# Optimization experiments

Hardware: AMD Instinct MI355X
Metric: run time of the kernel (lower is better)

## Reference

```python
import jax, jax.numpy as jnp
import numpy as np

B, FRAMES, IMG, PATCH = 2, 4, 224, 16
D_MODEL, D_INNER, D_STATE, DT_RANK, DEPTH, D_CONV = 256, 512, 16, 16, 12, 4
NPATCH = (IMG // PATCH) ** 2  # 196


def setup_inputs() -> dict:
    keys = iter(jax.random.split(jax.random.key(0), 80))

    def n(shape, s=0.02):
        return jax.random.normal(next(keys), shape, dtype=jnp.float32) * s

    A_init = jnp.broadcast_to(jnp.log(jnp.arange(1, D_STATE + 1, dtype=jnp.float32)), (DEPTH, D_INNER, D_STATE))
    inp = {
        'x': jax.random.normal(next(keys), (B, 3, FRAMES, IMG, IMG), dtype=jnp.float32),
        'patch_w': n((D_MODEL, 3, 1, PATCH, PATCH)),
        'patch_b': jnp.zeros((D_MODEL,), jnp.float32),
        'pos_embed': n((1, NPATCH, D_MODEL)),
        'temp_pos': n((1, FRAMES, D_MODEL)),
        'in_proj_w': n((DEPTH, 2 * D_INNER, D_MODEL), D_MODEL ** -0.5),
        'convf_w': n((DEPTH, D_INNER, D_CONV), 0.3),
        'convf_b': jnp.zeros((DEPTH, D_INNER), jnp.float32),
        'xprojf_w': n((DEPTH, DT_RANK + 2 * D_STATE, D_INNER), D_INNER ** -0.5),
        'dtf_w': n((DEPTH, D_INNER, DT_RANK), DT_RANK ** -0.5),
        'dtf_b': jnp.full((DEPTH, D_INNER), -4.6, jnp.float32) + n((DEPTH, D_INNER), 0.1),
        'A_logf': A_init,
        'Dsf': jnp.ones((DEPTH, D_INNER), jnp.float32),
        'convb_w': n((DEPTH, D_INNER, D_CONV), 0.3),
        'convb_b': jnp.zeros((DEPTH, D_INNER), jnp.float32),
        'xprojb_w': n((DEPTH, DT_RANK + 2 * D_STATE, D_INNER), D_INNER ** -0.5),
        'dtb_w': n((DEPTH, D_INNER, DT_RANK), DT_RANK ** -0.5),
        'dtb_b': jnp.full((DEPTH, D_INNER), -4.6, jnp.float32) + n((DEPTH, D_INNER), 0.1),
        'A_logb': A_init,
        'Dsb': jnp.ones((DEPTH, D_INNER), jnp.float32),
        'out_proj_w': n((DEPTH, D_MODEL, D_INNER), D_INNER ** -0.5),
        'norm_w': jnp.ones((DEPTH, D_MODEL), jnp.float32),
        'normf_w': jnp.ones((D_MODEL,), jnp.float32),
        'bbox_w1': n((D_MODEL, D_MODEL), D_MODEL ** -0.5),
        'bbox_b1': jnp.zeros((D_MODEL,), jnp.float32),
        'bbox_w2': n((3, D_MODEL), D_MODEL ** -0.5),
        'bbox_b2': jnp.zeros((3,), jnp.float32),
        'pix_w1': n((4, D_MODEL, D_MODEL), D_MODEL ** -0.5),
        'pix_b1': jnp.zeros((4, D_MODEL), jnp.float32),
        'pix_w2': n((4, 2, D_MODEL), D_MODEL ** -0.5),
        'pix_b2': jnp.zeros((4, 2), jnp.float32),
    }
    return inp


def rmsnorm(x, w, eps=1e-5):
    x = x.astype(jnp.float32)
    return x * jax.lax.rsqrt(jnp.mean(x * x, axis=-1, keepdims=True) + eps) * w


def ssm_scan(u, dt, A, Bm, Cm):
    # u, dt: [B,L,di]; Bm, Cm: [B,L,st]; A: [di,st]
    def step(h, inp):
        dt_t, B_t, C_t, u_t = inp  # [B,di],[B,st],[B,st],[B,di]
        h = jnp.exp(dt_t[..., None] * A) * h + (dt_t * u_t)[..., None] * B_t[:, None, :]
        return h, jnp.einsum('bds,bs->bd', h, C_t)
    h0 = jnp.zeros((u.shape[0], u.shape[2], A.shape[1]), u.dtype)
    xs = (dt.swapaxes(0, 1), Bm.swapaxes(0, 1), Cm.swapaxes(0, 1), u.swapaxes(0, 1))
    _, ys = jax.lax.scan(step, h0, xs)
    return ys.swapaxes(0, 1)  # [B,L,di]


def mamba_dir(x, z, cw, cb, xpw, dtw, dtb, A_log, Ds):
    L = x.shape[1]
    xp = jnp.pad(x, ((0, 0), (D_CONV - 1, 0), (0, 0)))  # causal depthwise conv
    xc = cb + sum(xp[:, k:k + L, :] * cw[:, k] for k in range(D_CONV))
    xs = jax.nn.silu(xc)
    dbl = xs @ xpw.T  # [B,L,dt_rank+2*st]
    dt = jax.nn.softplus(dbl[..., :DT_RANK] @ dtw.T + dtb)
    Bm = dbl[..., DT_RANK:DT_RANK + D_STATE]
    Cm = dbl[..., DT_RANK + D_STATE:]
    y = ssm_scan(xs, dt, -jnp.exp(A_log), Bm, Cm) + Ds * xs
    return y * jax.nn.silu(z)


def _forward(x, patch_w, patch_b, pos_embed, temp_pos, in_proj_w, convf_w, convf_b, xprojf_w, dtf_w, dtf_b, A_logf, Dsf, convb_w, convb_b, xprojb_w, dtb_w, dtb_b, A_logb, Dsb, out_proj_w, norm_w, normf_w, bbox_w1, bbox_b1, bbox_w2, bbox_b2, pix_w1, pix_b1, pix_w2, pix_b2):
    feat = jax.lax.conv_general_dilated(x, patch_w, (1, PATCH, PATCH), 'VALID', dimension_numbers=('NCDHW', 'OIDHW', 'NCDHW'))
    feat = feat + patch_b[None, :, None, None, None]
    b, c, t, h, w = feat.shape
    np_ = h * w
    tok = feat.transpose(0, 2, 3, 4, 1).reshape(b * t, np_, c) + pos_embed
    tok = tok.reshape(b, t, np_, c).transpose(0, 2, 1, 3).reshape(b * np_, t, c) + temp_pos
    tok = tok.reshape(b, np_, t, c).transpose(0, 2, 1, 3).reshape(b, t * np_, c)
    hidden, residual = tok, None
    for i in range(DEPTH):
        residual = hidden if residual is None else hidden + residual  # fused add+norm (prenorm)
        hidden = rmsnorm(residual, norm_w[i])
        xz = hidden @ in_proj_w[i].T
        xi, zi = jnp.split(xz, 2, axis=-1)
        yf = mamba_dir(xi, zi, convf_w[i], convf_b[i], xprojf_w[i], dtf_w[i], dtf_b[i], A_logf[i], Dsf[i])
        yb = mamba_dir(xi[:, ::-1], zi[:, ::-1], convb_w[i], convb_b[i], xprojb_w[i], dtb_w[i], dtb_b[i], A_logb[i], Dsb[i])[:, ::-1]
        hidden = (yf + yb) @ out_proj_w[i].T
    residual = hidden + residual
    hidden = rmsnorm(residual, normf_w)
    fus = hidden[:, :5, :]  # [B,5,hidden_dim] fusion_output for DETR head
    bbox = jax.nn.relu(fus[:, 0] @ bbox_w1.T + bbox_b1) @ bbox_w2.T + bbox_b2  # [B,3]
    pix = jnp.stack([jax.nn.sigmoid(jax.nn.relu(fus[:, i + 1] @ pix_w1[i].T + pix_b1[i]) @ pix_w2[i].T + pix_b2[i]) for i in range(4)], axis=1)  # [B,4,2]
    return jnp.concatenate([bbox, pix.reshape(bbox.shape[0], 8)], axis=-1)  # [B,11]


def reference(x, patch_w, patch_b, pos_embed, temp_pos, in_proj_w, convf_w, convf_b, xprojf_w, dtf_w, dtf_b, A_logf, Dsf, convb_w, convb_b, xprojb_w, dtb_w, dtb_b, A_logb, Dsb, out_proj_w, norm_w, normf_w, bbox_w1, bbox_b1, bbox_w2, bbox_b2, pix_w1, pix_b1, pix_w2, pix_b2):
    return _forward(x, patch_w, patch_b, pos_embed, temp_pos, in_proj_w, convf_w, convf_b, xprojf_w, dtf_w, dtf_b, A_logf, Dsf, convb_w, convb_b, xprojb_w, dtb_w, dtb_b, A_logb, Dsb, out_proj_w, norm_w, normf_w, bbox_w1, bbox_b1, bbox_w2, bbox_b2, pix_w1, pix_b1, pix_w2, pix_b2)
```

## Files before the change

kernel.cpp:

```cpp
#include <hip/hip_runtime.h>
#include <hip/hip_bf16.h>
#include <cmath>

#define BB 2
#define TT 4
#define NPATCH 196
#define LL 784
#define CC 256
#define DI 512
#define NSTATE 16
#define DEPTH 12
#define NCHUNK 49
#define CLEN 16
#define CTAU 8

typedef short short8 __attribute__((ext_vector_type(8)));
typedef float f32x4 __attribute__((ext_vector_type(4)));

__device__ __forceinline__ float sigmoidf_(float x){ return 1.f/(1.f+__expf(-x)); }
__device__ __forceinline__ float siluf_(float x){ return x/(1.f+__expf(-x)); }
__device__ __forceinline__ float softplusf_(float x){ return x > 20.f ? x : log1pf(__expf(x)); }
__device__ __forceinline__ unsigned short f2bf(float f){
  union { float f; unsigned int u; } v; v.f = f;
  unsigned int u = v.u;
  return (unsigned short)((u + 0x7FFFu + ((u>>16)&1u)) >> 16);
}
__device__ __forceinline__ float bf2f(unsigned short u){
  union { unsigned int i; float f; } v; v.i = ((unsigned int)u)<<16; return v.f;
}

#define PREP_NA 3072
#define PREP_NB 1536
#define PREP_NC 192
#define PREP_ND 1536
#define PREP_NF 784
#define PREP_NG 4704
__global__ void k_prep_all(
    const float* __restrict__ in_proj, unsigned short* __restrict__ WinB,
    const float* __restrict__ out_proj, unsigned short* __restrict__ WoutB,
    const float* __restrict__ patch_w, unsigned short* __restrict__ WpB,
    const float* __restrict__ xpf, const float* __restrict__ xpb, unsigned short* __restrict__ Wxp,
    const float* __restrict__ pb, const float* __restrict__ pos, const float* __restrict__ tpos,
    float* __restrict__ PB,
    const float* __restrict__ x, unsigned short* __restrict__ XCol)
{
  int blk = blockIdx.x;
  if (blk < PREP_NA + PREP_NB + PREP_NC) {
    const float* src; unsigned short* dst; int i;
    if (blk < PREP_NA)                  { src = in_proj;  dst = WinB;  i = blk*256 + threadIdx.x; }
    else if (blk < PREP_NA + PREP_NB)   { src = out_proj; dst = WoutB; i = (blk-PREP_NA)*256 + threadIdx.x; }
    else                                { src = patch_w;  dst = WpB;   i = (blk-PREP_NA-PREP_NB)*256 + threadIdx.x; }
    float4 v = *(const float4*)(src + (size_t)i*4);
    unsigned short o[4] = { f2bf(v.x), f2bf(v.y), f2bf(v.z), f2bf(v.w) };
    *(uint2*)(dst + (size_t)i*4) = *(uint2*)o;
    return;
  }
  blk -= PREP_NA + PREP_NB + PREP_NC;
  if (blk < PREP_ND) {
    int r = blk & 63; int ld = blk >> 6;
    int layer = ld >> 1, dir = ld & 1;
    const float* src = dir ? xpb : xpf;
    for (int kk = threadIdx.x; kk < 512; kk += 256) {
      float v = (r < 48) ? src[((size_t)layer*48 + r)*512 + kk] : 0.f;
      Wxp[((size_t)blk)*512 + kk] = f2bf(v);
    }
    return;
  }
  blk -= PREP_ND;
  if (blk < PREP_NF) {
    int tp = blk;
    int t = tp / NPATCH, p = tp - t*NPATCH;
    int c = threadIdx.x;
    PB[(size_t)tp*CC + c] = pb[c] + pos[(size_t)p*CC + c] + tpos[(size_t)t*CC + c];
    return;
  }
  blk -= PREP_NF;
  {
    int ci = blk / (BB*LL);
    int row = blk - ci*(BB*LL);
    int b = row / LL, rem = row - b*LL;
    int t = rem / NPATCH, p = rem - t*NPATCH;
    int ph = p / 14, pc = p - ph*14;
    int ii = threadIdx.x >> 4, jj = threadIdx.x & 15;
    float v = x[(((size_t)(b*3+ci)*TT + t)*224 + (ph*16+ii))*224 + (pc*16+jj)];
    XCol[(size_t)row*768 + ci*256 + threadIdx.x] = f2bf(v);
  }
}

__global__ __launch_bounds__(256) void k_gemm_mfma(
    const unsigned short* __restrict__ Ab, const unsigned short* __restrict__ Ab2,
    const unsigned short* __restrict__ Wb,
    float* __restrict__ Out, unsigned short* __restrict__ Outb,
    const float* __restrict__ bias, int M, int Nn, int K)
{
  __shared__ short As[64][40];
  __shared__ short Bs[64][40];
  int bm = blockIdx.x*64, bn = blockIdx.y*64;
  int tid = threadIdx.x;
  int wave = tid>>6, lane = tid&63;
  int wm = (wave>>1)*32, wn = (wave&1)*32;
  int quad = lane>>4, l16 = lane&15;
  f32x4 acc[2][2];
  #pragma unroll
  for (int i=0;i<2;i++)
    #pragma unroll
    for (int j=0;j<2;j++){ acc[i][j][0]=0.f; acc[i][j][1]=0.f; acc[i][j][2]=0.f; acc[i][j][3]=0.f; }
  int sr = tid>>2, sc = (tid&3)<<3;
  int gr = bm + sr;
  for (int k0 = 0; k0 < K; k0 += 32) {
    short8 av = {0,0,0,0,0,0,0,0};
    if (gr < M) {
      av = *(const short8*)(Ab + (size_t)gr*K + k0 + sc);
      if (Ab2) {
        short8 a2v = *(const short8*)(Ab2 + (size_t)gr*K + k0 + sc);
        #pragma unroll
        for (int j=0;j<8;j++)
          av[j] = (short)f2bf(bf2f((unsigned short)av[j]) + bf2f((unsigned short)a2v[j]));
      }
    }
    *(short8*)&As[sr][sc] = av;
    short8 bv = *(const short8*)(Wb + (size_t)(bn+sr)*K + k0 + sc);
    *(short8*)&Bs[sr][sc] = bv;
    __syncthreads();
    short8 a0 = *(const short8*)&As[wm    +l16][quad<<3];
    short8 a1 = *(const short8*)&As[wm+16+l16][quad<<3];
    short8 b0 = *(const short8*)&Bs[wn    +l16][quad<<3];
    short8 b1 = *(const short8*)&Bs[wn+16+l16][quad<<3];
    acc[0][0] = __builtin_amdgcn_mfma_f32_16x16x32_bf16(a0,b0,acc[0][0],0,0,0);
    acc[0][1] = __builtin_amdgcn_mfma_f32_16x16x32_bf16(a0,b1,acc[0][1],0,0,0);
    acc[1][0] = __builtin_amdgcn_mfma_f32_16x16x32_bf16(a1,b0,acc[1][0],0,0,0);
    acc[1][1] = __builtin_amdgcn_mfma_f32_16x16x32_bf16(a1,b1,acc[1][1],0,0,0);
    __syncthreads();
  }
  #pragma unroll
  for (int i=0;i<2;i++){
    #pragma unroll
    for (int r=0;r<4;r++){
      int row = bm + wm + i*16 + quad*4 + r;
      if (row < M) {
        #pragma unroll
        for (int j=0;j<2;j++){
          int col = bn + wn + j*16 + l16;
          float vv = acc[i][j][r];
          if (bias) vv += bias[(size_t)(row % LL)*Nn + col];
          if (Outb) Outb[(size_t)row*Nn + col] = f2bf(vv);
          else      Out [(size_t)row*Nn + col] = vv;
        }
      }
    }
  }
}

__global__ __launch_bounds__(256) void k_gemm_xp(
    const unsigned short* __restrict__ XSb, const unsigned short* __restrict__ Wxp,
    float* __restrict__ DBL)
{
  __shared__ short As[64][40];
  __shared__ short Bs[64][40];
  int z = blockIdx.z;
  int bm = blockIdx.x*64;
  const unsigned short* A = XSb + (size_t)z*2*LL*DI;
  const unsigned short* W = Wxp + (size_t)z*64*DI;
  int tid = threadIdx.x;
  int wave = tid>>6, lane = tid&63;
  int wm = (wave>>1)*32, wn = (wave&1)*32;
  int quad = lane>>4, l16 = lane&15;
  f32x4 acc[2][2];
  #pragma unroll
  for (int i=0;i<2;i++)
    #pragma unroll
    for (int j=0;j<2;j++){ acc[i][j][0]=0.f; acc[i][j][1]=0.f; acc[i][j][2]=0.f; acc[i][j][3]=0.f; }
  int sr = tid>>2, sc = (tid&3)<<3;
  int gr = bm + sr;
  for (int k0 = 0; k0 < DI; k0 += 32) {
    short8 av = {0,0,0,0,0,0,0,0};
    if (gr < 2*LL) av = *(const short8*)(A + (size_t)gr*DI + k0 + sc);
    *(short8*)&As[sr][sc] = av;
    *(short8*)&Bs[sr][sc] = *(const short8*)(W + (size_t)sr*DI + k0 + sc);
    __syncthreads();
    short8 a0 = *(const short8*)&As[wm    +l16][quad<<3];
    short8 a1 = *(const short8*)&As[wm+16+l16][quad<<3];
    short8 b0 = *(const short8*)&Bs[wn    +l16][quad<<3];
    short8 b1 = *(const short8*)&Bs[wn+16+l16][quad<<3];
    acc[0][0] = __builtin_amdgcn_mfma_f32_16x16x32_bf16(a0,b0,acc[0][0],0,0,0);
    acc[0][1] = __builtin_amdgcn_mfma_f32_16x16x32_bf16(a0,b1,acc[0][1],0,0,0);
    acc[1][0] = __builtin_amdgcn_mfma_f32_16x16x32_bf16(a1,b0,acc[1][0],0,0,0);
    acc[1][1] = __builtin_amdgcn_mfma_f32_16x16x32_bf16(a1,b1,acc[1][1],0,0,0);
    __syncthreads();
  }
  #pragma unroll
  for (int i=0;i<2;i++){
    #pragma unroll
    for (int r=0;r<4;r++){
      int row = bm + wm + i*16 + quad*4 + r;
      if (row < 2*LL) {
        size_t grow = (size_t)z*2*LL + row;
        #pragma unroll
        for (int j=0;j<2;j++){
          int col = wn + j*16 + l16;
          DBL[grow*64 + col] = acc[i][j][r];
        }
      }
    }
  }
}

__global__ void k_conv_silu(const unsigned short* __restrict__ XZb,
    const float* __restrict__ cwf, const float* __restrict__ cbf,
    const float* __restrict__ cwb, const float* __restrict__ cbb,
    unsigned short* __restrict__ XSb)
{
  int dir = blockIdx.z;
  int blk = blockIdx.x;
  int b = blk / (LL/CTAU), tq = blk - b*(LL/CTAU);
  int t0 = tq * CTAU;
  const float* cw = dir ? cwb : cwf;
  const float* cb = dir ? cbb : cbf;
  int d = threadIdx.x;
  float4 w4 = *(const float4*)(cw + (size_t)d*4);
  float bia = cb[d];
  const unsigned short* xz = XZb + (size_t)b*LL*1024 + d;
  float x0 = 0.f, x1 = 0.f, x2 = 0.f;
  {
    int tt = t0-3; if (tt >= 0) x0 = bf2f(xz[(size_t)(dir ? (LL-1-tt) : tt)*1024]);
    tt = t0-2;     if (tt >= 0) x1 = bf2f(xz[(size_t)(dir ? (LL-1-tt) : tt)*1024]);
    tt = t0-1;     if (tt >= 0) x2 = bf2f(xz[(size_t)(dir ? (LL-1-tt) : tt)*1024]);
  }
  size_t rowbase = ((size_t)(dir*BB + b)*LL + t0)*DI + d;
  #pragma unroll
  for (int i = 0; i < CTAU; ++i) {
    int tt = t0 + i;
    int torig = dir ? (LL-1-tt) : tt;
    float xin = bf2f(xz[(size_t)torig*1024]);
    float acc = bia;
    acc = fmaf(x0, w4.x, acc);
    acc = fmaf(x1, w4.y, acc);
    acc = fmaf(x2, w4.z, acc);
    acc = fmaf(xin, w4.w, acc);
    XSb[rowbase + (size_t)i*DI] = f2bf(siluf_(acc));
    x0 = x1; x1 = x2; x2 = xin;
  }
}

__global__ void k_res_rms(const float* __restrict__ Hin, float* __restrict__ R,
                          unsigned short* __restrict__ Nout, const float* __restrict__ w, int first)
{
  int row = blockIdx.x, c = threadIdx.x;
  size_t idx = (size_t)row*CC + c;
  float h = Hin[idx];
  float r = first ? h : (h + R[idx]);
  R[idx] = r;
  float v = r*r;
  #pragma unroll
  for (int m=1;m<64;m<<=1) v += __shfl_xor(v,m);
  __shared__ float sred[4];
  if ((c & 63)==0) sred[c>>6]=v;
  __syncthreads();
  float tot = sred[0]+sred[1]+sred[2]+sred[3];
  float sc = rsqrtf(tot*(1.f/CC) + 1e-5f);
  Nout[idx] = f2bf(r*sc*w[c]);
}

__global__ void k_scan1(const unsigned short* __restrict__ XSb, const float* __restrict__ DBL,
                        const float* __restrict__ dtwf, const float* __restrict__ dtwb,
                        const float* __restrict__ dtbf, const float* __restrict__ dtbb,
                        const float* __restrict__ Alf, const float* __restrict__ Alb,
                        float* __restrict__ Pb, float* __restrict__ Hcb)
{
  int chunk = blockIdx.x;
  int d = blockIdx.y*256 + threadIdx.x;
  int dirb = blockIdx.z;
  int dir = dirb >> 1;
  const float* Al = dir ? Alb : Alf;
  const float* dtw = dir ? dtwb : dtwf;
  float dtbv = (dir ? dtbb : dtbf)[d];
  float a2[NSTATE], wd[NSTATE];
  {
    const float4* ar = (const float4*)(Al + (size_t)d*NSTATE);
    const float4* wr = (const float4*)(dtw + (size_t)d*NSTATE);
    #pragma unroll
    for (int q=0;q<4;q++){
      float4 v = ar[q];
      a2[q*4+0] = -__expf(v.x)*1.44269504f;
      a2[q*4+1] = -__expf(v.y)*1.44269504f;
      a2[q*4+2] = -__expf(v.z)*1.44269504f;
      a2[q*4+3] = -__expf(v.w)*1.44269504f;
      float4 w = wr[q];
      wd[q*4+0] = w.x; wd[q*4+1] = w.y; wd[q*4+2] = w.z; wd[q*4+3] = w.w;
    }
  }
  __shared__ float Dl[CLEN][NSTATE], Bl[CLEN][NSTATE];
  {
    int t = threadIdx.x >> 4, s = threadIdx.x & 15;
    size_t row = ((size_t)dirb*LL + chunk*CLEN + t)*64;
    Dl[t][s] = DBL[row + s];
    Bl[t][s] = DBL[row + 16 + s];
  }
  __syncthreads();
  size_t base = (size_t)dirb*LL*DI;
  const unsigned short* xs = XSb + base + (size_t)chunk*CLEN*DI + d;
  float P[NSTATE], h[NSTATE];
  #pragma unroll
  for (int s=0;s<NSTATE;s++){ P[s]=1.f; h[s]=0.f; }
  for (int i = 0; i < CLEN; ++i) {
    float dtv = dtbv;
    #pragma unroll
    for (int r=0;r<NSTATE;r++) dtv = fmaf(Dl[i][r], wd[r], dtv);
    float dt = softplusf_(dtv);
    float u  = bf2f(xs[(size_t)i*DI]);
    float du = dt*u;
    #pragma unroll
    for (int s=0;s<NSTATE;s++){
      float e = exp2f(dt*a2[s]);
      P[s] *= e;
      h[s] = fmaf(e, h[s], du*Bl[i][s]);
    }
  }
  size_t ob = ((size_t)dirb*NCHUNK + chunk)*NSTATE*DI + d;
  #pragma unroll
  for (int s=0;s<NSTATE;s++){
    Pb [ob + (size_t)s*DI] = P[s];
    Hcb[ob + (size_t)s*DI] = h[s];
  }
}

__global__ void k_scan2(const float* __restrict__ Pb, float* __restrict__ Hcb)
{
  int i = blockIdx.x*256 + threadIdx.x;
  int dirb = blockIdx.y;
  float h = 0.f;
  for (int c = 0; c < NCHUNK; ++c) {
    size_t idx = ((size_t)dirb*NCHUNK + c)*NSTATE*DI + i;
    float p = Pb[idx], hl = Hcb[idx];
    Hcb[idx] = h;
    h = fmaf(p, h, hl);
  }
}

__global__ void k_scan3(const unsigned short* __restrict__ XSb, const float* __restrict__ DBL,
                        const unsigned short* __restrict__ XZb,
                        const float* __restrict__ dtwf, const float* __restrict__ dtwb,
                        const float* __restrict__ dtbf, const float* __restrict__ dtbb,
                        const float* __restrict__ Alf, const float* __restrict__ Alb,
                        const float* __restrict__ Dsfp, const float* __restrict__ Dsbp,
                        const float* __restrict__ Hcb, unsigned short* __restrict__ Yb)
{
  int chunk = blockIdx.x;
  int d = blockIdx.y*256 + threadIdx.x;
  int dirb = blockIdx.z;
  int dir = dirb >> 1, b = dirb & 1;
  const float* Al = dir ? Alb : Alf;
  const float* dtw = dir ? dtwb : dtwf;
  float dtbv = (dir ? dtbb : dtbf)[d];
  float a2[NSTATE], wd[NSTATE];
  {
    const float4* ar = (const float4*)(Al + (size_t)d*NSTATE);
    const float4* wr = (const float4*)(dtw + (size_t)d*NSTATE);
    #pragma unroll
    for (int q=0;q<4;q++){
      float4 v = ar[q];
      a2[q*4+0] = -__expf(v.x)*1.44269504f;
      a2[q*4+1] = -__expf(v.y)*1.44269504f;
      a2[q*4+2] = -__expf(v.z)*1.44269504f;
      a2[q*4+3] = -__expf(v.w)*1.44269504f;
      float4 w = wr[q];
      wd[q*4+0] = w.x; wd[q*4+1] = w.y; wd[q*4+2] = w.z; wd[q*4+3] = w.w;
    }
  }
  __shared__ float Dl[CLEN][NSTATE];
  __shared__ float BCl[CLEN][32];
  {
    int t = threadIdx.x >> 4, s = threadIdx.x & 15;
    size_t row = ((size_t)dirb*LL + chunk*CLEN + t)*64;
    Dl[t][s] = DBL[row + s];
    BCl[t][s] = DBL[row + 16 + s];
    BCl[t][16+s] = DBL[row + 32 + s];
  }
  __syncthreads();
  float h[NSTATE];
  size_t ob = ((size_t)dirb*NCHUNK + chunk)*NSTATE*DI + d;
  #pragma unroll
  for (int s=0;s<NSTATE;s++) h[s] = Hcb[ob + (size_t)s*DI];
  float Dsv = (dir ? Dsbp : Dsfp)[d];
  size_t base = (size_t)dirb*LL*DI;
  const unsigned short* xs = XSb + base + (size_t)chunk*CLEN*DI + d;
  const unsigned short* zpb = XZb + (size_t)b*LL*1024 + 512 + d;
  unsigned short* y = Yb + base + d;
  for (int i = 0; i < CLEN; ++i) {
    int tau = chunk*CLEN + i;
    float dtv = dtbv;
    #pragma unroll
    for (int r=0;r<NSTATE;r++) dtv = fmaf(Dl[i][r], wd[r], dtv);
    float dt = softplusf_(dtv);
    float u  = bf2f(xs[(size_t)i*DI]);
    float du = dt*u;
    float yacc = 0.f;
    #pragma unroll
    for (int s=0;s<NSTATE;s++){
      float e = exp2f(dt*a2[s]);
      h[s] = fmaf(e, h[s], du*BCl[i][s]);
      yacc = fmaf(h[s], BCl[i][16+s], yacc);
    }
    int torig = dir ? (LL-1-tau) : tau;
    float zv = bf2f(zpb[(size_t)torig*1024]);
    y[(size_t)torig*DI] = f2bf((yacc + Dsv*u) * siluf_(zv));
  }
}

__global__ void k_head(const float* __restrict__ H, const float* __restrict__ R,
                       const float* __restrict__ nw,
                       const float* __restrict__ bw1, const float* __restrict__ bb1,
                       const float* __restrict__ bw2, const float* __restrict__ bb2,
                       const float* __restrict__ pw1, const float* __restrict__ pb1,
                       const float* __restrict__ pw2, const float* __restrict__ pb2,
                       float* __restrict__ out)
{
  int b = blockIdx.x / 5, j = blockIdx.x % 5;
  int c = threadIdx.x;
  __shared__ float fus[CC], h1[CC];
  __shared__ float sred[4];
  size_t idx = ((size_t)b*LL + j)*CC + c;
  float r = H[idx] + R[idx];
  float v = r*r;
  #pragma unroll
  for (int m=1;m<64;m<<=1) v += __shfl_xor(v,m);
  if ((c&63)==0) sred[c>>6]=v;
  __syncthreads();
  float tot = sred[0]+sred[1]+sred[2]+sred[3];
  fus[c] = r * rsqrtf(tot*(1.f/CC)+1e-5f) * nw[c];
  __syncthreads();
  const float* W1 = (j==0) ? bw1 : (pw1 + (size_t)(j-1)*CC*CC);
  const float* B1 = (j==0) ? bb1 : (pb1 + (j-1)*CC);
  float a = B1[c];
  for (int k=0;k<CC;k++) a = fmaf(fus[k], W1[(size_t)c*CC+k], a);
  h1[c] = fmaxf(a, 0.f);
  __syncthreads();
  if (j==0) {
    if (c < 3) {
      float o = bb2[c];
      for (int k=0;k<CC;k++) o = fmaf(h1[k], bw2[c*CC+k], o);
      out[b*11 + c] = o;
    }
  } else {
    if (c < 2) {
      const float* W2 = pw2 + (size_t)((j-1)*2 + c)*CC;
      float o = pb2[(j-1)*2 + c];
      for (int k=0;k<CC;k++) o = fmaf(h1[k], W2[k], o);
      out[b*11 + 3 + (j-1)*2 + c] = sigmoidf_(o);
    }
  }
}

extern "C" void kernel_launch(void* const* d_in, const int* in_sizes, int n_in,
                              void* d_out, int out_size, void* d_ws, size_t ws_size,
                              hipStream_t stream)
{
  const float* x        = (const float*)d_in[0];
  const float* patch_w  = (const float*)d_in[1];
  const float* patch_b  = (const float*)d_in[2];
  const float* pos      = (const float*)d_in[3];
  const float* tpos     = (const float*)d_in[4];
  const float* in_proj  = (const float*)d_in[5];
  const float* convf_w  = (const float*)d_in[6];
  const float* convf_b  = (const float*)d_in[7];
  const float* xprojf_w = (const float*)d_in[8];
  const float* dtf_w    = (const float*)d_in[9];
  const float* dtf_b    = (const float*)d_in[10];
  const float* A_logf   = (const float*)d_in[11];
  const float* Dsf      = (const float*)d_in[12];
  const float* convb_w  = (const float*)d_in[13];
  const float* convb_b  = (const float*)d_in[14];
  const float* xprojb_w = (const float*)d_in[15];
  const float* dtb_w    = (const float*)d_in[16];
  const float* dtb_b    = (const float*)d_in[17];
  const float* A_logb   = (const float*)d_in[18];
  const float* Dsb      = (const float*)d_in[19];
  const float* out_proj = (const float*)d_in[20];
  const float* norm_w   = (const float*)d_in[21];
  const float* normf_w  = (const float*)d_in[22];
  const float* bbox_w1  = (const float*)d_in[23];
  const float* bbox_b1  = (const float*)d_in[24];
  const float* bbox_w2  = (const float*)d_in[25];
  const float* bbox_b2  = (const float*)d_in[26];
  const float* pix_w1   = (const float*)d_in[27];
  const float* pix_b1   = (const float*)d_in[28];
  const float* pix_w2   = (const float*)d_in[29];
  const float* pix_b2   = (const float*)d_in[30];
  float* out = (float*)d_out;

  float* ws = (float*)d_ws;
  const size_t nTok = (size_t)BB*LL;
  float* H   = ws;                 ws += nTok*CC;
  float* R   = ws;                 ws += nTok*CC;
  float* DBL = ws;                 ws += 2*nTok*64;
  float* Pb  = ws;                 ws += (size_t)4*NCHUNK*NSTATE*DI;
  float* Hcb = ws;                 ws += (size_t)4*NCHUNK*NSTATE*DI;
  float* PB  = ws;                 ws += (size_t)LL*CC;
  unsigned short* WinB  = (unsigned short*)ws;  ws += (size_t)DEPTH*1024*CC/2;
  unsigned short* WoutB = (unsigned short*)ws;  ws += (size_t)DEPTH*CC*DI/2;
  unsigned short* WpB   = (unsigned short*)ws;  ws += (size_t)CC*768/2;
  unsigned short* XCol  = (unsigned short*)ws;  ws += nTok*768/2;
  unsigned short* NrmB  = (unsigned short*)ws;  ws += nTok*CC/2;
  unsigned short* XZb   = (unsigned short*)ws;  ws += nTok*1024/2;
  unsigned short* XSb   = (unsigned short*)ws;  ws += 2*nTok*DI/2;
  unsigned short* Yb    = (unsigned short*)ws;  ws += 2*nTok*DI/2;
  unsigned short* Wxp   = (unsigned short*)ws;  ws += (size_t)DEPTH*2*64*DI/2;
  (void)ws_size; (void)in_sizes; (void)n_in; (void)out_size;

  {
    const unsigned prepBlocks = PREP_NA + PREP_NB + PREP_NC + PREP_ND + PREP_NF + PREP_NG;
    k_prep_all<<<dim3(prepBlocks), 256, 0, stream>>>(
        in_proj, WinB, out_proj, WoutB, patch_w, WpB,
        xprojf_w, xprojb_w, Wxp,
        patch_b, pos, tpos, PB, x, XCol);
  }
  k_gemm_mfma<<<dim3(25, 4), 256, 0, stream>>>(XCol, nullptr, WpB, H, nullptr, PB,
                                               (int)nTok, CC, 768);

  for (int i = 0; i < DEPTH; ++i) {
    k_res_rms<<<dim3((unsigned)nTok), 256, 0, stream>>>(H, R, NrmB, norm_w + i*CC, i==0 ? 1 : 0);
    k_gemm_mfma<<<dim3(25, 16), 256, 0, stream>>>(NrmB, nullptr,
        WinB + (size_t)i*1024*CC, nullptr, XZb, nullptr, (int)nTok, 1024, CC);
    k_conv_silu<<<dim3(BB*LL/CTAU, 1, 2), DI, 0, stream>>>(XZb,
        convf_w + (size_t)i*DI*4, convf_b + (size_t)i*DI,
        convb_w + (size_t)i*DI*4, convb_b + (size_t)i*DI, XSb);
    k_gemm_xp<<<dim3(25, 1, 2), 256, 0, stream>>>(XSb,
        Wxp + (size_t)i*2*64*DI, DBL);
    k_scan1<<<dim3(NCHUNK, 2, 4), 256, 0, stream>>>(XSb, DBL,
        dtf_w + (size_t)i*DI*16, dtb_w + (size_t)i*DI*16,
        dtf_b + (size_t)i*DI, dtb_b + (size_t)i*DI,
        A_logf + (size_t)i*DI*NSTATE, A_logb + (size_t)i*DI*NSTATE, Pb, Hcb);
    k_scan2<<<dim3(32, 4), 256, 0, stream>>>(Pb, Hcb);
    k_scan3<<<dim3(NCHUNK, 2, 4), 256, 0, stream>>>(XSb, DBL, XZb,
        dtf_w + (size_t)i*DI*16, dtb_w + (size_t)i*DI*16,
        dtf_b + (size_t)i*DI, dtb_b + (size_t)i*DI,
        A_logf + (size_t)i*DI*NSTATE, A_logb + (size_t)i*DI*NSTATE,
        Dsf + (size_t)i*DI, Dsb + (size_t)i*DI, Hcb, Yb);
    k_gemm_mfma<<<dim3(25, 4), 256, 0, stream>>>(Yb, Yb + nTok*DI,
        WoutB + (size_t)i*CC*DI, H, nullptr, nullptr, (int)nTok, CC, DI);
  }
  k_head<<<dim3(10), 256, 0, stream>>>(H, R, normf_w, bbox_w1, bbox_b1, bbox_w2, bbox_b2,
                                       pix_w1, pix_b1, pix_w2, pix_b2, out);
}
```

Measured before the change: 1.212 ms.

## Fuse residual add and RMSNorm into the out-proj and in-proj GEMMs

```diff
diff --git a/kernel.cpp b/kernel.cpp
--- a/kernel.cpp
+++ b/kernel.cpp
@@ -35,6 +35,7 @@
 #define PREP_ND 1536
 #define PREP_NF 784
 #define PREP_NG 4704
+#define PREP_NH 80
 __global__ void k_prep_all(
     const float* __restrict__ in_proj, unsigned short* __restrict__ WinB,
     const float* __restrict__ out_proj, unsigned short* __restrict__ WoutB,
@@ -42,7 +43,8 @@
     const float* __restrict__ xpf, const float* __restrict__ xpb, unsigned short* __restrict__ Wxp,
     const float* __restrict__ pb, const float* __restrict__ pos, const float* __restrict__ tpos,
     float* __restrict__ PB,
-    const float* __restrict__ x, unsigned short* __restrict__ XCol)
+    const float* __restrict__ x, unsigned short* __restrict__ XCol,
+    float* __restrict__ SS)
 {
   int blk = blockIdx.x;
   if (blk < PREP_NA + PREP_NB + PREP_NC) {
@@ -75,7 +77,7 @@
     return;
   }
   blk -= PREP_NF;
-  {
+  if (blk < PREP_NG) {
     int ci = blk / (BB*LL);
     int row = blk - ci*(BB*LL);
     int b = row / LL, rem = row - b*LL;
@@ -84,14 +86,21 @@
     int ii = threadIdx.x >> 4, jj = threadIdx.x & 15;
     float v = x[(((size_t)(b*3+ci)*TT + t)*224 + (ph*16+ii))*224 + (pc*16+jj)];
     XCol[(size_t)row*768 + ci*256 + threadIdx.x] = f2bf(v);
-  }
-}
-
-__global__ __launch_bounds__(256) void k_gemm_mfma(
+    return;
+  }
+  blk -= PREP_NG;
+  {
+    int i = blk*256 + threadIdx.x;
+    if (i < 13*BB*LL) SS[i] = 0.f;
+  }
+}
+
+__global__ __launch_bounds__(256) void k_gemm_res(
     const unsigned short* __restrict__ Ab, const unsigned short* __restrict__ Ab2,
     const unsigned short* __restrict__ Wb,
-    float* __restrict__ Out, unsigned short* __restrict__ Outb,
-    const float* __restrict__ bias, int M, int Nn, int K)
+    const float* __restrict__ bias, const float* __restrict__ Rold,
+    float* __restrict__ Rnew, unsigned short* __restrict__ RnewB,
+    float* __restrict__ SS, int M, int Nn, int K)
 {
   __shared__ short As[64][40];
   __shared__ short Bs[64][40];
@@ -119,8 +128,7 @@
       }
     }
     *(short8*)&As[sr][sc] = av;
-    short8 bv = *(const short8*)(Wb + (size_t)(bn+sr)*K + k0 + sc);
-    *(short8*)&Bs[sr][sc] = bv;
+    *(short8*)&Bs[sr][sc] = *(const short8*)(Wb + (size_t)(bn+sr)*K + k0 + sc);
     __syncthreads();
     short8 a0 = *(const short8*)&As[wm    +l16][quad<<3];
     short8 a1 = *(const short8*)&As[wm+16+l16][quad<<3];
@@ -137,14 +145,84 @@
     #pragma unroll
     for (int r=0;r<4;r++){
       int row = bm + wm + i*16 + quad*4 + r;
+      float s = 0.f;
       if (row < M) {
         #pragma unroll
         for (int j=0;j<2;j++){
           int col = bn + wn + j*16 + l16;
           float vv = acc[i][j][r];
           if (bias) vv += bias[(size_t)(row % LL)*Nn + col];
-          if (Outb) Outb[(size_t)row*Nn + col] = f2bf(vv);
-          else      Out [(size_t)row*Nn + col] = vv;
+          if (Rold) vv += Rold[(size_t)row*Nn + col];
+          Rnew [(size_t)row*Nn + col] = vv;
+          RnewB[(size_t)row*Nn + col] = f2bf(vv);
+          s += vv*vv;
+        }
+      }
+      s += __shfl_xor(s,1); s += __shfl_xor(s,2); s += __shfl_xor(s,4); s += __shfl_xor(s,8);
+      if (row < M && l16 == 0) atomicAdd(&SS[row], s);
+    }
+  }
+}
+
+__global__ __launch_bounds__(256) void k_gemm_in(
+    const unsigned short* __restrict__ RnewB, const float* __restrict__ SS,
+    const float* __restrict__ normw, const unsigned short* __restrict__ Wb,
+    unsigned short* __restrict__ Outb, int M)
+{
+  __shared__ short As[64][40];
+  __shared__ short Bs[64][40];
+  int bm = blockIdx.x*64, bn = blockIdx.y*64;
+  int tid = threadIdx.x;
+  int wave = tid>>6, lane = tid&63;
+  int wm = (wave>>1)*32, wn = (wave&1)*32;
+  int quad = lane>>4, l16 = lane&15;
+  f32x4 acc[2][2];
+  #pragma unroll
+  for (int i=0;i<2;i++)
+    #pragma unroll
+    for (int j=0;j<2;j++){ acc[i][j][0]=0.f; acc[i][j][1]=0.f; acc[i][j][2]=0.f; acc[i][j][3]=0.f; }
+  int sr = tid>>2, sc = (tid&3)<<3;
+  int gr = bm + sr;
+  float sc_row = 0.f;
+  if (gr < M) sc_row = rsqrtf(SS[gr]*(1.f/CC) + 1e-5f);
+  for (int k0 = 0; k0 < CC; k0 += 32) {
+    short8 av = {0,0,0,0,0,0,0,0};
+    if (gr < M) {
+      short8 rb = *(const short8*)(RnewB + (size_t)gr*CC + k0 + sc);
+      float4 w0 = *(const float4*)(normw + k0 + sc);
+      float4 w1 = *(const float4*)(normw + k0 + sc + 4);
+      av[0] = (short)f2bf(bf2f((unsigned short)rb[0]) * sc_row * w0.x);
+      av[1] = (short)f2bf(bf2f((unsigned short)rb[1]) * sc_row * w0.y);
+      av[2] = (short)f2bf(bf2f((unsigned short)rb[2]) * sc_row * w0.z);
+      av[3] = (short)f2bf(bf2f((unsigned short)rb[3]) * sc_row * w0.w);
+      av[4] = (short)f2bf(bf2f((unsigned short)rb[4]) * sc_row * w1.x);
+      av[5] = (short)f2bf(bf2f((unsigned short)rb[5]) * sc_row * w1.y);
+      av[6] = (short)f2bf(bf2f((unsigned short)rb[6]) * sc_row * w1.z);
+      av[7] = (short)f2bf(bf2f((unsigned short)rb[7]) * sc_row * w1.w);
+    }
+    *(short8*)&As[sr][sc] = av;
+    *(short8*)&Bs[sr][sc] = *(const short8*)(Wb + (size_t)(bn+sr)*CC + k0 + sc);
+    __syncthreads();
+    short8 a0 = *(const short8*)&As[wm    +l16][quad<<3];
+    short8 a1 = *(const short8*)&As[wm+16+l16][quad<<3];
+    short8 b0 = *(const short8*)&Bs[wn    +l16][quad<<3];
+    short8 b1 = *(const short8*)&Bs[wn+16+l16][quad<<3];
+    acc[0][0] = __builtin_amdgcn_mfma_f32_16x16x32_bf16(a0,b0,acc[0][0],0,0,0);
+    acc[0][1] = __builtin_amdgcn_mfma_f32_16x16x32_bf16(a0,b1,acc[0][1],0,0,0);
+    acc[1][0] = __builtin_amdgcn_mfma_f32_16x16x32_bf16(a1,b0,acc[1][0],0,0,0);
+    acc[1][1] = __builtin_amdgcn_mfma_f32_16x16x32_bf16(a1,b1,acc[1][1],0,0,0);
+    __syncthreads();
+  }
+  #pragma unroll
+  for (int i=0;i<2;i++){
+    #pragma unroll
+    for (int r=0;r<4;r++){
+      int row = bm + wm + i*16 + quad*4 + r;
+      if (row < M) {
+        #pragma unroll
+        for (int j=0;j<2;j++){
+          int col = bn + wn + j*16 + l16;
+          Outb[(size_t)row*1024 + col] = f2bf(acc[i][j][r]);
         }
       }
     }
@@ -242,25 +320,6 @@
   }
 }
 
-__global__ void k_res_rms(const float* __restrict__ Hin, float* __restrict__ R,
-                          unsigned short* __restrict__ Nout, const float* __restrict__ w, int first)
-{
-  int row = blockIdx.x, c = threadIdx.x;
-  size_t idx = (size_t)row*CC + c;
-  float h = Hin[idx];
-  float r = first ? h : (h + R[idx]);
-  R[idx] = r;
-  float v = r*r;
-  #pragma unroll
-  for (int m=1;m<64;m<<=1) v += __shfl_xor(v,m);
-  __shared__ float sred[4];
-  if ((c & 63)==0) sred[c>>6]=v;
-  __syncthreads();
-  float tot = sred[0]+sred[1]+sred[2]+sred[3];
-  float sc = rsqrtf(tot*(1.f/CC) + 1e-5f);
-  Nout[idx] = f2bf(r*sc*w[c]);
-}
-
 __global__ void k_scan1(const unsigned short* __restrict__ XSb, const float* __restrict__ DBL,
                         const float* __restrict__ dtwf, const float* __restrict__ dtwb,
                         const float* __restrict__ dtbf, const float* __restrict__ dtbb,
@@ -407,7 +466,7 @@
   }
 }
 
-__global__ void k_head(const float* __restrict__ H, const float* __restrict__ R,
+__global__ void k_head(const float* __restrict__ Rf,
                        const float* __restrict__ nw,
                        const float* __restrict__ bw1, const float* __restrict__ bb1,
                        const float* __restrict__ bw2, const float* __restrict__ bb2,
@@ -420,7 +479,7 @@
   __shared__ float fus[CC], h1[CC];
   __shared__ float sred[4];
   size_t idx = ((size_t)b*LL + j)*CC + c;
-  float r = H[idx] + R[idx];
+  float r = Rf[idx];
   float v = r*r;
   #pragma unroll
   for (int m=1;m<64;m<<=1) v += __shfl_xor(v,m);
@@ -490,37 +549,40 @@
 
   float* ws = (float*)d_ws;
   const size_t nTok = (size_t)BB*LL;
-  float* H   = ws;                 ws += nTok*CC;
-  float* R   = ws;                 ws += nTok*CC;
+  float* Rb0 = ws;                 ws += nTok*CC;
+  float* Rb1 = ws;                 ws += nTok*CC;
   float* DBL = ws;                 ws += 2*nTok*64;
   float* Pb  = ws;                 ws += (size_t)4*NCHUNK*NSTATE*DI;
   float* Hcb = ws;                 ws += (size_t)4*NCHUNK*NSTATE*DI;
   float* PB  = ws;                 ws += (size_t)LL*CC;
+  float* SS  = ws;                 ws += (size_t)(DEPTH+1)*nTok;
   unsigned short* WinB  = (unsigned short*)ws;  ws += (size_t)DEPTH*1024*CC/2;
   unsigned short* WoutB = (unsigned short*)ws;  ws += (size_t)DEPTH*CC*DI/2;
   unsigned short* WpB   = (unsigned short*)ws;  ws += (size_t)CC*768/2;
   unsigned short* XCol  = (unsigned short*)ws;  ws += nTok*768/2;
-  unsigned short* NrmB  = (unsigned short*)ws;  ws += nTok*CC/2;
+  unsigned short* RbB0  = (unsigned short*)ws;  ws += nTok*CC/2;
+  unsigned short* RbB1  = (unsigned short*)ws;  ws += nTok*CC/2;
   unsigned short* XZb   = (unsigned short*)ws;  ws += nTok*1024/2;
   unsigned short* XSb   = (unsigned short*)ws;  ws += 2*nTok*DI/2;
   unsigned short* Yb    = (unsigned short*)ws;  ws += 2*nTok*DI/2;
   unsigned short* Wxp   = (unsigned short*)ws;  ws += (size_t)DEPTH*2*64*DI/2;
+  float* Rbuf[2] = { Rb0, Rb1 };
+  unsigned short* RbBuf[2] = { RbB0, RbB1 };
   (void)ws_size; (void)in_sizes; (void)n_in; (void)out_size;
 
   {
-    const unsigned prepBlocks = PREP_NA + PREP_NB + PREP_NC + PREP_ND + PREP_NF + PREP_NG;
+    const unsigned prepBlocks = PREP_NA + PREP_NB + PREP_NC + PREP_ND + PREP_NF + PREP_NG + PREP_NH;
     k_prep_all<<<dim3(prepBlocks), 256, 0, stream>>>(
         in_proj, WinB, out_proj, WoutB, patch_w, WpB,
         xprojf_w, xprojb_w, Wxp,
-        patch_b, pos, tpos, PB, x, XCol);
-  }
-  k_gemm_mfma<<<dim3(25, 4), 256, 0, stream>>>(XCol, nullptr, WpB, H, nullptr, PB,
-                                               (int)nTok, CC, 768);
+        patch_b, pos, tpos, PB, x, XCol, SS);
+  }
+  k_gemm_res<<<dim3(25, 4), 256, 0, stream>>>(XCol, nullptr, WpB, PB, nullptr,
+      Rbuf[0], RbBuf[0], SS, (int)nTok, CC, 768);
 
   for (int i = 0; i < DEPTH; ++i) {
-    k_res_rms<<<dim3((unsigned)nTok), 256, 0, stream>>>(H, R, NrmB, norm_w + i*CC, i==0 ? 1 : 0);
-    k_gemm_mfma<<<dim3(25, 16), 256, 0, stream>>>(NrmB, nullptr,
-        WinB + (size_t)i*1024*CC, nullptr, XZb, nullptr, (int)nTok, 1024, CC);
+    k_gemm_in<<<dim3(25, 16), 256, 0, stream>>>(RbBuf[i & 1], SS + (size_t)i*nTok,
+        norm_w + i*CC, WinB + (size_t)i*1024*CC, XZb, (int)nTok);
     k_conv_silu<<<dim3(BB*LL/CTAU, 1, 2), DI, 0, stream>>>(XZb,
         convf_w + (size_t)i*DI*4, convf_b + (size_t)i*DI,
         convb_w + (size_t)i*DI*4, convb_b + (size_t)i*DI, XSb);
@@ -536,9 +598,11 @@
         dtf_b + (size_t)i*DI, dtb_b + (size_t)i*DI,
         A_logf + (size_t)i*DI*NSTATE, A_logb + (size_t)i*DI*NSTATE,
         Dsf + (size_t)i*DI, Dsb + (size_t)i*DI, Hcb, Yb);
-    k_gemm_mfma<<<dim3(25, 4), 256, 0, stream>>>(Yb, Yb + nTok*DI,
-        WoutB + (size_t)i*CC*DI, H, nullptr, nullptr, (int)nTok, CC, DI);
-  }
-  k_head<<<dim3(10), 256, 0, stream>>>(H, R, normf_w, bbox_w1, bbox_b1, bbox_w2, bbox_b2,
+    k_gemm_res<<<dim3(25, 4), 256, 0, stream>>>(Yb, Yb + nTok*DI,
+        WoutB + (size_t)i*CC*DI, nullptr, Rbuf[i & 1],
+        Rbuf[(i + 1) & 1], RbBuf[(i + 1) & 1], SS + (size_t)(i + 1)*nTok,
+        (int)nTok, CC, DI);
+  }
+  k_head<<<dim3(10), 256, 0, stream>>>(Rbuf[0], normf_w, bbox_w1, bbox_b1, bbox_w2, bbox_b2,
                                        pix_w1, pix_b1, pix_w2, pix_b2, out);
 }
```

Measured after the change: 1.258 ms. 1.04x slower.
